# Kernel optimization log

Hardware: AMD Instinct MI355X
Metric: run time of the kernel (lower is better)

The kernel has to match this reference:

```python
import jax, jax.numpy as jnp
import numpy as np

B, T, DM, H, DK, N_STEPS = 4, 1024, 1024, 16, 64, 3


def setup_inputs() -> dict:
    key = jax.random.key(0)
    ks = jax.random.split(key, 8)
    s = 1.0 / np.sqrt(DM).astype(np.float32)
    x = jax.random.normal(ks[0], (B, T, DM), jnp.float32)
    W_Q = jax.random.normal(ks[1], (DM, DM), jnp.float32) * s
    W_K = jax.random.normal(ks[2], (DM, DM), jnp.float32) * s
    W_re = jax.random.normal(ks[3], (DM, DM), jnp.float32) * s
    W_im = jax.random.normal(ks[4], (DM, DM), jnp.float32) * s
    W_V = jax.random.normal(ks[5], (DM, DM), jnp.float32) * s
    W_O = jax.random.normal(ks[6], (DM, DM), jnp.float32) * s
    logit_lam = jnp.float32(0.0)  # sigmoid(0)=0.5 == cfg.lam
    return {"x": x, "W_Q": W_Q, "W_K": W_K, "W_re": W_re, "W_im": W_im,
            "W_V": W_V, "W_O": W_O, "logit_lam": logit_lam}


def _heads(y):
    # (B,T,DM) -> (B,H,T,DK)
    return y.reshape(B, T, H, DK).transpose(0, 2, 1, 3)


def reference(x, W_Q, W_K, W_re, W_im, W_V, W_O, logit_lam):
    # AdjacencyBuilder: soft row-normalized adjacency
    Q = _heads(x @ W_Q)
    K = _heads(x @ W_K)
    scores = jnp.einsum('bhtd,bhsd->bhts', Q, K) / jnp.float32(np.sqrt(DK))
    A = jax.nn.softmax(scores, axis=-1)                      # (B,H,T,T)
    # PhaseEncoding: complex oscillator versors
    D = jax.lax.complex(_heads(x @ W_re), _heads(x @ W_im))  # (B,H,T,DK) c64
    # TopologyPropagation: D <- (1-lam) D + lam A D, n_steps times
    lam = jax.nn.sigmoid(logit_lam)
    A_c = A.astype(jnp.complex64)
    for _ in range(N_STEPS):
        D = (1.0 - lam) * D + lam * jnp.einsum('bhts,bhsd->bhtd', A_c, D)
    # CollapseReadout (phase_align): softmax over T of cosine to mean field
    mean_D = jnp.mean(D, axis=-2, keepdims=True)             # (B,H,1,DK)
    dot = (D * jnp.conj(mean_D)).real
    norm = jnp.abs(D) * jnp.abs(mean_D) + 1e-8
    gate = jax.nn.softmax(dot / norm, axis=-2)               # (B,H,T,DK)
    # Value gating + output projection (dropout is identity in eval)
    V = _heads(x @ W_V)
    out = (gate * V).transpose(0, 2, 1, 3).reshape(B, T, DM) @ W_O
    return out, gate
```

## Files before the change

kernel.cpp:

```cpp
#include <hip/hip_runtime.h>
#include <math.h>

#define Bc 4
#define Tc 1024
#define DMc 1024
#define Hc 16
#define DKc 64
#define BHc 64
#define Mc 4096
#define TD (Tc*DKc)
#define TD2 (Tc*128)
#define TDS (128*2048)

typedef __bf16 bf16_t;
typedef bf16_t bf16x4 __attribute__((ext_vector_type(4)));
typedef bf16_t bf16x8 __attribute__((ext_vector_type(8)));
typedef float  f32x4  __attribute__((ext_vector_type(4)));

#define KLSTR 136
#define DLSTR 72

__device__ __forceinline__ bf16x8 ld8(const bf16_t* p) {
    return *(const bf16x8*)p;
}
__device__ __forceinline__ void packsplit4(bf16_t* dh, bf16_t* dl, float4 v) {
    bf16x4 h, l;
    h[0]=(bf16_t)v.x; l[0]=(bf16_t)(v.x-(float)h[0]);
    h[1]=(bf16_t)v.y; l[1]=(bf16_t)(v.y-(float)h[1]);
    h[2]=(bf16_t)v.z; l[2]=(bf16_t)(v.z-(float)h[2]);
    h[3]=(bf16_t)v.w; l[3]=(bf16_t)(v.w-(float)h[3]);
    *(bf16x4*)dh = h; *(bf16x4*)dl = l;
}
__device__ __forceinline__ unsigned pk2(bf16_t a, bf16_t b) {
    unsigned short ua = __builtin_bit_cast(unsigned short, a);
    unsigned short ub = __builtin_bit_cast(unsigned short, b);
    return (unsigned)ua | ((unsigned)ub << 16);
}
__device__ __forceinline__ void gload16(const bf16_t* g, bf16_t* l) {
    __builtin_amdgcn_global_load_lds(
        (__attribute__((address_space(1))) void*)(bf16_t*)g,
        (__attribute__((address_space(3))) void*)l, 16, 0, 0);
}

__global__ __launch_bounds__(256)
void convx_k(const float* __restrict__ x,
             bf16_t* __restrict__ xh, bf16_t* __restrict__ xl)
{
    size_t i = ((size_t)blockIdx.x * 256 + threadIdx.x) * 4;
    float4 v = *(const float4*)&x[i];
    packsplit4(&xh[i], &xl[i], v);
}

__global__ __launch_bounds__(256)
void convw_k(const float* __restrict__ W0, const float* __restrict__ W1,
             const float* __restrict__ W2, const float* __restrict__ W3,
             const float* __restrict__ W4, const float* __restrict__ W5,
             bf16_t* __restrict__ WT)
{
    __shared__ float tile[32][33];
    const float* Ws[6] = {W0, W1, W2, W3, W4, W5};
    const int wi = blockIdx.z;
    const float* W = Ws[wi];
    bf16_t* WTh = WT + (size_t)wi * 2097152;
    bf16_t* WTl = WTh + 1048576;

    const int tx = threadIdx.x & 31, ty = threadIdx.x >> 5;
    const int k0 = blockIdx.x * 32, n0 = blockIdx.y * 32;
#pragma unroll
    for (int i = 0; i < 4; i++)
        tile[ty + 8*i][tx] = W[(size_t)(k0 + ty + 8*i) * DMc + n0 + tx];
    __syncthreads();
    const int kg = threadIdx.x & 7, n = threadIdx.x >> 3;
    float4 v = make_float4(tile[kg*4+0][n], tile[kg*4+1][n],
                           tile[kg*4+2][n], tile[kg*4+3][n]);
    const size_t o = (size_t)(n0 + n) * DMc + k0 + kg*4;
    packsplit4(&WTh[o], &WTl[o], v);
}

template<int MODE>
__global__ __launch_bounds__(256)
void mgemm_k(const bf16_t* __restrict__ Ah, const bf16_t* __restrict__ Al,
             const bf16_t* __restrict__ WT,
             bf16_t* __restrict__ Oq, bf16_t* __restrict__ Ok,
             bf16_t* __restrict__ Od, float* __restrict__ Ov,
             float* __restrict__ Of)
{
    __shared__ bf16_t S[4][128*32];

    const int tid = threadIdx.x;
    const int wv  = tid >> 6;
    const int ln  = tid & 63;
    const int l15 = ln & 15;
    const int qd  = ln >> 4;
    const int m0  = blockIdx.x * 128;
    const int by  = blockIdx.y;

    const bf16_t *Bh, *Bl;
    int n0, sel, kt0, kt1;
    float* Opart;
    if (MODE == 0) {
        sel = by >> 3;
        n0 = (by & 7) * 128;
        Bh = WT + (size_t)sel * 2097152;
        Bl = Bh + 1048576;
        kt0 = 0; kt1 = DMc;
        Opart = nullptr;
    } else {
        sel = 5;
        Bh = WT + (size_t)5 * 2097152;
        Bl = Bh + 1048576;
        n0 = by * 128;
        kt0 = blockIdx.z * 256; kt1 = kt0 + 256;
        Opart = Of + (size_t)blockIdx.z * ((size_t)Mc * DMc);
    }

    const int srow = ln >> 2;
    const int scol = (ln & 3) * 8;
    const bf16_t* sbase;
    if (wv == 0)      sbase = Ah + (size_t)(m0 + srow) * DMc + scol;
    else if (wv == 1) sbase = Al + (size_t)(m0 + srow) * DMc + scol;
    else if (wv == 2) sbase = Bh + (size_t)(n0 + srow) * DMc + scol;
    else              sbase = Bl + (size_t)(n0 + srow) * DMc + scol;
    sbase += kt0;
    bf16_t* ldst = &S[wv][0];

    f32x4 acc[4][4];
#pragma unroll
    for (int i = 0; i < 4; i++)
#pragma unroll
        for (int j = 0; j < 4; j++) acc[i][j] = (f32x4)0.f;

#pragma unroll 1
    for (int kt = kt0; kt < kt1; kt += 32) {
        __syncthreads();
#pragma unroll
        for (int i = 0; i < 8; i++)
            gload16(sbase + (size_t)i * 16 * DMc, ldst + i * 512);
        sbase += 32;
        __syncthreads();

        bf16x8 fah[4], fal[4], fbh[4], fbl[4];
#pragma unroll
        for (int it = 0; it < 4; it++) {
            const int row = ((wv>>1)*64 + it*16 + l15) * 32 + qd*8;
            fah[it] = *(const bf16x8*)&S[0][row];
            fal[it] = *(const bf16x8*)&S[1][row];
        }
#pragma unroll
        for (int jt = 0; jt < 4; jt++) {
            const int row = ((wv&1)*64 + jt*16 + l15) * 32 + qd*8;
            fbh[jt] = *(const bf16x8*)&S[2][row];
            fbl[jt] = *(const bf16x8*)&S[3][row];
        }
#pragma unroll
        for (int it = 0; it < 4; it++)
#pragma unroll
            for (int jt = 0; jt < 4; jt++) {
                acc[it][jt] = __builtin_amdgcn_mfma_f32_16x16x32_bf16(
                    fah[it], fbh[jt], acc[it][jt], 0, 0, 0);
                acc[it][jt] = __builtin_amdgcn_mfma_f32_16x16x32_bf16(
                    fah[it], fbl[jt], acc[it][jt], 0, 0, 0);
                acc[it][jt] = __builtin_amdgcn_mfma_f32_16x16x32_bf16(
                    fal[it], fbh[jt], acc[it][jt], 0, 0, 0);
            }
    }

#pragma unroll
    for (int it = 0; it < 4; it++) {
        const int mb = m0 + (wv>>1)*64 + it*16 + qd*4;
#pragma unroll
        for (int jt = 0; jt < 4; jt++) {
            const int col = n0 + (wv&1)*64 + jt*16 + l15;
            if (MODE == 0) {
                const int hh = col >> 6;
                const int b  = mb >> 10, t0 = mb & 1023;
                if (sel <= 1) {
                    bf16_t* O = sel ? Ok : Oq;
                    const int d = col & 63;
#pragma unroll
                    for (int r = 0; r < 4; r++) {
                        const float val = acc[it][jt][r];
                        const size_t o = ((size_t)(b*Hc + hh)*Tc + t0 + r)*128 + d;
                        bf16_t vh = (bf16_t)val;
                        O[o]      = vh;
                        O[o + 64] = (bf16_t)(val - (float)vh);
                    }
                } else if (sel <= 3) {
                    const int d = (sel == 3 ? 64 : 0) + (col & 63);
                    bf16x4 h4, l4;
#pragma unroll
                    for (int r = 0; r < 4; r++) {
                        const float val = acc[it][jt][r];
                        h4[r] = (bf16_t)val;
                        l4[r] = (bf16_t)(val - (float)h4[r]);
                    }
                    const size_t o = (size_t)(b*Hc + hh)*TDS + (size_t)d*2048 + t0;
                    *(bf16x4*)&Od[o]        = h4;
                    *(bf16x4*)&Od[o + 1024] = l4;
                } else {
#pragma unroll
                    for (int r = 0; r < 4; r++)
                        Ov[((size_t)(b*Hc + hh)*Tc + t0 + r)*64 + (col & 63)]
                            = acc[it][jt][r];
                }
            } else {
#pragma unroll
                for (int r = 0; r < 4; r++)
                    Opart[(size_t)(mb + r) * DMc + col] = acc[it][jt][r];
            }
        }
    }
}

__global__ __launch_bounds__(256)
void reduce4_k(const float* __restrict__ p0, const float* __restrict__ p1,
               const float* __restrict__ p2, const float* __restrict__ p3,
               float* __restrict__ out)
{
    size_t i = ((size_t)blockIdx.x * 256 + threadIdx.x) * 4;
    float4 a = *(const float4*)&p0[i];
    float4 b = *(const float4*)&p1[i];
    float4 c = *(const float4*)&p2[i];
    float4 d = *(const float4*)&p3[i];
    *(float4*)&out[i] = make_float4(a.x+b.x+c.x+d.x, a.y+b.y+c.y+d.y,
                                    a.z+b.z+c.z+d.z, a.w+b.w+c.w+d.w);
}

template<int FINAL>
__global__ __launch_bounds__(256)
void prop_k(const bf16_t* __restrict__ Qg, const bf16_t* __restrict__ Kg,
            const bf16_t* __restrict__ DTin, bf16_t* __restrict__ DTout,
            float* __restrict__ Dc, const float* __restrict__ llam)
{
    __shared__ bf16_t Ks[32*KLSTR];
    __shared__ bf16_t Ds[128*DLSTR];

    const int tid = threadIdx.x;
    const int wv  = tid >> 6;
    const int ln  = tid & 63;
    const int l15 = ln & 15;
    const int qd  = ln >> 4;
    const int bh  = blockIdx.x;
    const int Tw  = blockIdx.y * 128 + wv * 32;

    const bf16_t* Qh  = Qg   + (size_t)bh * (Tc*128);
    const bf16_t* Kh  = Kg   + (size_t)bh * (Tc*128);
    const bf16_t* DTh = DTin + (size_t)bh * TDS;

    bf16x8 qfh[2][2], qfl[2][2];
#pragma unroll
    for (int tj = 0; tj < 2; tj++) {
        const bf16_t* qp = &Qh[(size_t)(Tw + tj*16 + l15) * 128];
#pragma unroll
        for (int ks = 0; ks < 2; ks++) {
            qfh[tj][ks] = *(const bf16x8*)&qp[ks*32 + qd*8];
            qfl[tj][ks] = *(const bf16x8*)&qp[64 + ks*32 + qd*8];
        }
    }

    const int idk0 = tid, idk1 = tid + 256;
    const bf16_t* srcK0 = Kh + (size_t)(idk0 >> 4) * 128 + (idk0 & 15) * 8;
    const bf16_t* srcK1 = Kh + (size_t)(idk1 >> 4) * 128 + (idk1 & 15) * 8;
    bf16_t* dstK0 = &Ks[(idk0 >> 4) * KLSTR + (idk0 & 15) * 8];
    bf16_t* dstK1 = &Ks[(idk1 >> 4) * KLSTR + (idk1 & 15) * 8];
    const bf16_t* srcD[4];
    bf16_t* dstD[4];
#pragma unroll
    for (int i = 0; i < 4; i++) {
        const int id = tid + i * 256;
        const int r = id >> 3, sg = id & 7;
        srcD[i] = DTh + (size_t)r * 2048
                      + (sg < 4 ? sg * 8 : 1024 + (sg - 4) * 8);
        dstD[i] = (sg < 4) ? &Ds[r * DLSTR + sg * 8]
                           : &Ds[r * DLSTR + 32 + (sg - 4) * 8];
    }
    bf16x8 kr0 = *(const bf16x8*)srcK0;
    bf16x8 kr1 = *(const bf16x8*)srcK1;
    bf16x8 dr[4];
#pragma unroll
    for (int i = 0; i < 4; i++) dr[i] = *(const bf16x8*)srcD[i];

    f32x4 acc[8][2];
#pragma unroll
    for (int i = 0; i < 8; i++)
#pragma unroll
        for (int j = 0; j < 2; j++) acc[i][j] = (f32x4)0.f;
    float rs[2] = {0.f, 0.f};

    const int srcA = (((qd & 1) * 2)     << 4) | l15;
    const int srcB = (((qd & 1) * 2 + 1) << 4) | l15;
    const bool loQuad = (qd < 2);

#pragma unroll 1
    for (int ch = 0; ch < 32; ch++) {
        __syncthreads();
        *(bf16x8*)dstK0 = kr0;
        *(bf16x8*)dstK1 = kr1;
#pragma unroll
        for (int i = 0; i < 4; i++) *(bf16x8*)dstD[i] = dr[i];
        __syncthreads();
        if (ch < 31) {
            kr0 = *(const bf16x8*)(srcK0 + (size_t)(ch + 1) * 4096);
            kr1 = *(const bf16x8*)(srcK1 + (size_t)(ch + 1) * 4096);
#pragma unroll
            for (int i = 0; i < 4; i++)
                dr[i] = *(const bf16x8*)(srcD[i] + (size_t)(ch + 1) * 32);
        }
        bf16x8 kfh[2][2], kfl[2][2];
#pragma unroll
        for (int si = 0; si < 2; si++) {
            const int row = (si*16 + l15) * KLSTR;
#pragma unroll
            for (int ks = 0; ks < 2; ks++) {
                kfh[si][ks] = ld8(&Ks[row + ks*32 + qd*8]);
                kfl[si][ks] = ld8(&Ks[row + 64 + ks*32 + qd*8]);
            }
        }
        f32x4 pacc[2][2];
#pragma unroll
        for (int si = 0; si < 2; si++)
#pragma unroll
            for (int tj = 0; tj < 2; tj++) pacc[si][tj] = (f32x4)0.f;
#pragma unroll
        for (int ks = 0; ks < 2; ks++)
#pragma unroll
            for (int si = 0; si < 2; si++)
#pragma unroll
                for (int tj = 0; tj < 2; tj++) {
                    pacc[si][tj] = __builtin_amdgcn_mfma_f32_16x16x32_bf16(
                        kfh[si][ks], qfh[tj][ks], pacc[si][tj], 0, 0, 0);
                    pacc[si][tj] = __builtin_amdgcn_mfma_f32_16x16x32_bf16(
                        kfl[si][ks], qfh[tj][ks], pacc[si][tj], 0, 0, 0);
                    pacc[si][tj] = __builtin_amdgcn_mfma_f32_16x16x32_bf16(
                        kfh[si][ks], qfl[tj][ks], pacc[si][tj], 0, 0, 0);
                }
        unsigned pk01h[2][2], pk23h[2][2], pk01l[2][2], pk23l[2][2];
#pragma unroll
        for (int si = 0; si < 2; si++)
#pragma unroll
            for (int tj = 0; tj < 2; tj++) {
                float e0 = __expf(pacc[si][tj][0] * 0.125f);
                float e1 = __expf(pacc[si][tj][1] * 0.125f);
                float e2 = __expf(pacc[si][tj][2] * 0.125f);
                float e3 = __expf(pacc[si][tj][3] * 0.125f);
                rs[tj] += (e0 + e1) + (e2 + e3);
                bf16_t h0=(bf16_t)e0, h1=(bf16_t)e1, h2=(bf16_t)e2, h3=(bf16_t)e3;
                pk01h[si][tj] = pk2(h0, h1);
                pk23h[si][tj] = pk2(h2, h3);
                pk01l[si][tj] = pk2((bf16_t)(e0-(float)h0), (bf16_t)(e1-(float)h1));
                pk23l[si][tj] = pk2((bf16_t)(e2-(float)h2), (bf16_t)(e3-(float)h3));
            }
        bf16x8 pfh[2], pfl[2];
#pragma unroll
        for (int tj = 0; tj < 2; tj++) {
            union { bf16x8 v; unsigned u[4]; } H, L;
            unsigned a0 = __shfl((int)pk01h[0][tj], srcA, 64);
            unsigned a1 = __shfl((int)pk23h[0][tj], srcA, 64);
            unsigned a2 = __shfl((int)pk01h[0][tj], srcB, 64);
            unsigned a3 = __shfl((int)pk23h[0][tj], srcB, 64);
            unsigned b0 = __shfl((int)pk01h[1][tj], srcA, 64);
            unsigned b1 = __shfl((int)pk23h[1][tj], srcA, 64);
            unsigned b2 = __shfl((int)pk01h[1][tj], srcB, 64);
            unsigned b3 = __shfl((int)pk23h[1][tj], srcB, 64);
            H.u[0] = loQuad ? a0 : b0;  H.u[1] = loQuad ? a1 : b1;
            H.u[2] = loQuad ? a2 : b2;  H.u[3] = loQuad ? a3 : b3;
            unsigned c0 = __shfl((int)pk01l[0][tj], srcA, 64);
            unsigned c1 = __shfl((int)pk23l[0][tj], srcA, 64);
            unsigned c2 = __shfl((int)pk01l[0][tj], srcB, 64);
            unsigned c3 = __shfl((int)pk23l[0][tj], srcB, 64);
            unsigned d0_ = __shfl((int)pk01l[1][tj], srcA, 64);
            unsigned d1 = __shfl((int)pk23l[1][tj], srcA, 64);
            unsigned d2 = __shfl((int)pk01l[1][tj], srcB, 64);
            unsigned d3 = __shfl((int)pk23l[1][tj], srcB, 64);
            L.u[0] = loQuad ? c0 : d0_; L.u[1] = loQuad ? c1 : d1;
            L.u[2] = loQuad ? c2 : d2;  L.u[3] = loQuad ? c3 : d3;
            pfh[tj] = H.v; pfl[tj] = L.v;
        }
#pragma unroll
        for (int half = 0; half < 2; half++) {
            bf16x8 dfh[4], dfl[4];
#pragma unroll
            for (int i = 0; i < 4; i++) {
                const int row = ((half*4 + i)*16 + l15) * DLSTR;
                dfh[i] = ld8(&Ds[row + qd*8]);
                dfl[i] = ld8(&Ds[row + 32 + qd*8]);
            }
#pragma unroll
            for (int i = 0; i < 4; i++)
#pragma unroll
                for (int tj = 0; tj < 2; tj++) {
                    acc[half*4+i][tj] = __builtin_amdgcn_mfma_f32_16x16x32_bf16(
                        dfh[i], pfh[tj], acc[half*4+i][tj], 0, 0, 0);
                    acc[half*4+i][tj] = __builtin_amdgcn_mfma_f32_16x16x32_bf16(
                        dfh[i], pfl[tj], acc[half*4+i][tj], 0, 0, 0);
                    acc[half*4+i][tj] = __builtin_amdgcn_mfma_f32_16x16x32_bf16(
                        dfl[i], pfh[tj], acc[half*4+i][tj], 0, 0, 0);
                }
        }
    }

#pragma unroll
    for (int tj = 0; tj < 2; tj++) {
        rs[tj] += __shfl_xor(rs[tj], 16);
        rs[tj] += __shfl_xor(rs[tj], 32);
    }

    const float lam = 1.f / (1.f + __expf(-llam[0]));
    const float oml = 1.f - lam;
    bf16_t* DToutg = (FINAL ? (bf16_t*)nullptr : DTout + (size_t)bh * TDS);

#pragma unroll
    for (int tj = 0; tj < 2; tj++) {
        const int t = Tw + tj*16 + l15;
        const float s = lam / rs[tj];
#pragma unroll
        for (int it = 0; it < 8; it++) {
            const int d0 = it*16 + qd*4;
            float v[4];
#pragma unroll
            for (int r = 0; r < 4; r++) {
                const size_t ro = (size_t)(d0 + r)*2048 + t;
                float res = (float)DTh[ro] + (float)DTh[ro + 1024];
                v[r] = oml*res + s*acc[it][tj][r];
            }
            if (FINAL) {
                *(float4*)&Dc[((size_t)bh*Tc + t)*128 + d0] =
                    make_float4(v[0], v[1], v[2], v[3]);
            } else {
#pragma unroll
                for (int r = 0; r < 4; r++) {
                    const size_t ro = (size_t)(d0 + r)*2048 + t;
                    bf16_t h = (bf16_t)v[r];
                    DToutg[ro]        = h;
                    DToutg[ro + 1024] = (bf16_t)(v[r] - (float)h);
                }
            }
        }
    }
}

__global__ __launch_bounds__(256)
void mean1_k(const float* __restrict__ D,
             float* __restrict__ M1re, float* __restrict__ M1im)
{
    __shared__ float sre[4][64], sim[4][64];
    const int bh = blockIdx.x, y = blockIdx.y;
    const int d = threadIdx.x & 63, q = threadIdx.x >> 6;
    const float* p = D + (size_t)bh * TD2;
    float ar = 0.f, ai = 0.f;
    const int t0 = y*128 + q*32;
    for (int t = t0; t < t0 + 32; t++) {
        ar += p[t*128 + d]; ai += p[t*128 + 64 + d];
    }
    sre[q][d] = ar; sim[q][d] = ai;
    __syncthreads();
    if (threadIdx.x < 64) {
        M1re[(bh*8 + y)*64 + d] = sre[0][d]+sre[1][d]+sre[2][d]+sre[3][d];
        M1im[(bh*8 + y)*64 + d] = sim[0][d]+sim[1][d]+sim[2][d]+sim[3][d];
    }
}

__global__ __launch_bounds__(64)
void mean2_k(const float* __restrict__ M1re, const float* __restrict__ M1im,
             float* __restrict__ Mre, float* __restrict__ Mim)
{
    const int bh = blockIdx.x, d = threadIdx.x;
    float r = 0.f, im = 0.f;
    for (int y = 0; y < 8; y++) {
        r  += M1re[(bh*8 + y)*64 + d];
        im += M1im[(bh*8 + y)*64 + d];
    }
    Mre[bh*64 + d] = r  * (1.f/1024.f);
    Mim[bh*64 + d] = im * (1.f/1024.f);
}

__global__ __launch_bounds__(256)
void gate1_k(const float* __restrict__ D,
             const float* __restrict__ Mre, const float* __restrict__ Mim,
             float* __restrict__ Gp)
{
    __shared__ float part[4][64];
    const int bh = blockIdx.x, y = blockIdx.y;
    const int d = threadIdx.x & 63, q = threadIdx.x >> 6;
    const float* p = D + (size_t)bh * TD2;
    const float mre = Mre[bh*64 + d], mim = Mim[bh*64 + d];
    const float mabs = sqrtf(mre*mre + mim*mim);

    float ps = 0.f;
    const int t0 = y*128 + q*32;
    for (int t = t0; t < t0 + 32; t++) {
        float dr = p[t*128 + d], dv = p[t*128 + 64 + d];
        float c = (dr*mre + dv*mim) / (sqrtf(dr*dr + dv*dv)*mabs + 1e-8f);
        ps += __expf(c);
    }
    part[q][d] = ps;
    __syncthreads();
    if (threadIdx.x < 64)
        Gp[(bh*8 + y)*64 + d] = part[0][d]+part[1][d]+part[2][d]+part[3][d];
}

__global__ __launch_bounds__(256)
void gate2_k(const float* __restrict__ D,
             const float* __restrict__ Mre, const float* __restrict__ Mim,
             const float* __restrict__ V, const float* __restrict__ Gp,
             float* __restrict__ gate_out,
             bf16_t* __restrict__ gVh, bf16_t* __restrict__ gVl)
{
    __shared__ float dinv[64];
    const int bh = blockIdx.x, y = blockIdx.y;
    const int d = threadIdx.x & 63, q = threadIdx.x >> 6;
    if (threadIdx.x < 64) {
        float s = 0.f;
        for (int yy = 0; yy < 8; yy++) s += Gp[(bh*8 + yy)*64 + d];
        dinv[d] = 1.f / s;
    }
    __syncthreads();

    const float* p = D + (size_t)bh * TD2;
    const float mre = Mre[bh*64 + d], mim = Mim[bh*64 + d];
    const float mabs = sqrtf(mre*mre + mim*mim);
    const float di_ = dinv[d];
    const int b = bh >> 4, hh = bh & 15;
    const float* pv = V + (size_t)bh * TD;
    const int t0 = y*128 + q*32;
    for (int t = t0; t < t0 + 32; t++) {
        float dr = p[t*128 + d], dv = p[t*128 + 64 + d];
        float c = (dr*mre + dv*mim) / (sqrtf(dr*dr + dv*dv)*mabs + 1e-8f);
        float g = __expf(c) * di_;
        gate_out[(size_t)bh*TD + t*64 + d] = g;
        float gv = g * pv[t*64 + d];
        size_t o = ((size_t)b*Tc + t)*DMc + hh*64 + d;
        bf16_t gh = (bf16_t)gv;
        gVh[o] = gh;
        gVl[o] = (bf16_t)(gv - (float)gh);
    }
}

extern "C" void kernel_launch(void* const* d_in, const int* in_sizes, int n_in,
                              void* d_out, int out_size, void* d_ws, size_t ws_size,
                              hipStream_t stream)
{
    const float* x    = (const float*)d_in[0];
    const float* W_Q  = (const float*)d_in[1];
    const float* W_K  = (const float*)d_in[2];
    const float* W_re = (const float*)d_in[3];
    const float* W_im = (const float*)d_in[4];
    const float* W_V  = (const float*)d_in[5];
    const float* W_O  = (const float*)d_in[6];
    const float* llam = (const float*)d_in[7];

    float* out      = (float*)d_out;
    float* gate_out = out + (size_t)Mc * DMc;

    float* ws = (float*)d_ws;
    const size_t M1 = 1024*1024;
    float*  Dc  = ws;
    bf16_t* DT1 = (bf16_t*)ws;
    bf16_t* DT0 = (bf16_t*)(ws + 8*M1);
    float*  V   = ws + 16*M1;
    bf16_t* Qs  = (bf16_t*)(ws + 20*M1);
    bf16_t* Ksb = (bf16_t*)(ws + 24*M1);
    float*  Mre = ws + 28*M1;
    float*  Mim = Mre + 4096;
    bf16_t* xh  = (bf16_t*)(ws + 28*M1 + 8192);
    bf16_t* xl  = xh + 4*M1;
    bf16_t* WT  = xl + 4*M1;
    bf16_t* gVh = xh;
    bf16_t* gVl = xl;
    float* Gp   = ws + 24*M1;
    float* M1re = Gp + 32768;
    float* M1im = M1re + 32768;
    float* P0 = ws + 8*M1;
    float* P1 = ws + 12*M1;
    float* P2 = ws + 16*M1;
    float* P3 = ws + 20*M1;

    convx_k<<<4096, 256, 0, stream>>>(x, xh, xl);
    convw_k<<<dim3(32, 32, 6), 256, 0, stream>>>(
        W_Q, W_K, W_re, W_im, W_V, W_O, WT);

    mgemm_k<0><<<dim3(32, 40), 256, 0, stream>>>(
        xh, xl, WT, Qs, Ksb, DT0, V, nullptr);

    prop_k<0><<<dim3(64, 8), 256, 0, stream>>>(Qs, Ksb, DT0, DT1, nullptr, llam);
    prop_k<0><<<dim3(64, 8), 256, 0, stream>>>(Qs, Ksb, DT1, DT0, nullptr, llam);
    prop_k<1><<<dim3(64, 8), 256, 0, stream>>>(Qs, Ksb, DT0, nullptr, Dc, llam);

    mean1_k<<<dim3(64, 8), 256, 0, stream>>>(Dc, M1re, M1im);
    mean2_k<<<64, 64, 0, stream>>>(M1re, M1im, Mre, Mim);
    gate1_k<<<dim3(64, 8), 256, 0, stream>>>(Dc, Mre, Mim, Gp);
    gate2_k<<<dim3(64, 8), 256, 0, stream>>>(Dc, Mre, Mim, V, Gp,
                                             gate_out, gVh, gVl);

    mgemm_k<1><<<dim3(32, 8, 4), 256, 0, stream>>>(
        gVh, gVl, WT, nullptr, nullptr, nullptr, nullptr, P0);
    reduce4_k<<<4096, 256, 0, stream>>>(P0, P1, P2, P3, out);
}
```

Baseline: 608.3 us.

## Load K and D fragments directly from global memory, dropping LDS staging

The propagation kernel no longer stages K and D tiles through shared memory with register prefetch and two barriers per chunk. Each wave now loads its MFMA operand fragments straight from global memory, relying on L1/L2 caching for the reuse across the four waves of a block. This removes barrier and LDS traffic, but it adds redundant global loads per wave and drops the software prefetch, which exposes load latency.

```diff
diff --git a/kernel.cpp b/kernel.cpp
--- a/kernel.cpp
+++ b/kernel.cpp
@@ -17,12 +17,6 @@
 typedef bf16_t bf16x8 __attribute__((ext_vector_type(8)));
 typedef float  f32x4  __attribute__((ext_vector_type(4)));
 
-#define KLSTR 136
-#define DLSTR 72
-
-__device__ __forceinline__ bf16x8 ld8(const bf16_t* p) {
-    return *(const bf16x8*)p;
-}
 __device__ __forceinline__ void packsplit4(bf16_t* dh, bf16_t* dl, float4 v) {
     bf16x4 h, l;
     h[0]=(bf16_t)v.x; l[0]=(bf16_t)(v.x-(float)h[0]);
@@ -232,9 +226,6 @@
             const bf16_t* __restrict__ DTin, bf16_t* __restrict__ DTout,
             float* __restrict__ Dc, const float* __restrict__ llam)
 {
-    __shared__ bf16_t Ks[32*KLSTR];
-    __shared__ bf16_t Ds[128*DLSTR];
-
     const int tid = threadIdx.x;
     const int wv  = tid >> 6;
     const int ln  = tid & 63;
@@ -258,27 +249,8 @@
         }
     }
 
-    const int idk0 = tid, idk1 = tid + 256;
-    const bf16_t* srcK0 = Kh + (size_t)(idk0 >> 4) * 128 + (idk0 & 15) * 8;
-    const bf16_t* srcK1 = Kh + (size_t)(idk1 >> 4) * 128 + (idk1 & 15) * 8;
-    bf16_t* dstK0 = &Ks[(idk0 >> 4) * KLSTR + (idk0 & 15) * 8];
-    bf16_t* dstK1 = &Ks[(idk1 >> 4) * KLSTR + (idk1 & 15) * 8];
-    const bf16_t* srcD[4];
-    bf16_t* dstD[4];
-#pragma unroll
-    for (int i = 0; i < 4; i++) {
-        const int id = tid + i * 256;
-        const int r = id >> 3, sg = id & 7;
-        srcD[i] = DTh + (size_t)r * 2048
-                      + (sg < 4 ? sg * 8 : 1024 + (sg - 4) * 8);
-        dstD[i] = (sg < 4) ? &Ds[r * DLSTR + sg * 8]
-                           : &Ds[r * DLSTR + 32 + (sg - 4) * 8];
-    }
-    bf16x8 kr0 = *(const bf16x8*)srcK0;
-    bf16x8 kr1 = *(const bf16x8*)srcK1;
-    bf16x8 dr[4];
-#pragma unroll
-    for (int i = 0; i < 4; i++) dr[i] = *(const bf16x8*)srcD[i];
+    const bf16_t* kbase = Kh + (size_t)l15 * 128 + qd * 8;
+    const bf16_t* dbase = DTh + (size_t)l15 * 2048 + qd * 8;
 
     f32x4 acc[8][2];
 #pragma unroll
@@ -293,27 +265,15 @@
 
 #pragma unroll 1
     for (int ch = 0; ch < 32; ch++) {
-        __syncthreads();
-        *(bf16x8*)dstK0 = kr0;
-        *(bf16x8*)dstK1 = kr1;
-#pragma unroll
-        for (int i = 0; i < 4; i++) *(bf16x8*)dstD[i] = dr[i];
-        __syncthreads();
-        if (ch < 31) {
-            kr0 = *(const bf16x8*)(srcK0 + (size_t)(ch + 1) * 4096);
-            kr1 = *(const bf16x8*)(srcK1 + (size_t)(ch + 1) * 4096);
-#pragma unroll
-            for (int i = 0; i < 4; i++)
-                dr[i] = *(const bf16x8*)(srcD[i] + (size_t)(ch + 1) * 32);
-        }
+        const int s0 = ch * 32;
         bf16x8 kfh[2][2], kfl[2][2];
 #pragma unroll
         for (int si = 0; si < 2; si++) {
-            const int row = (si*16 + l15) * KLSTR;
+            const bf16_t* kp = kbase + (size_t)(s0 + si*16) * 128;
 #pragma unroll
             for (int ks = 0; ks < 2; ks++) {
-                kfh[si][ks] = ld8(&Ks[row + ks*32 + qd*8]);
-                kfl[si][ks] = ld8(&Ks[row + 64 + ks*32 + qd*8]);
+                kfh[si][ks] = *(const bf16x8*)(kp + ks*32);
+                kfl[si][ks] = *(const bf16x8*)(kp + 64 + ks*32);
             }
         }
         f32x4 pacc[2][2];
@@ -381,9 +341,9 @@
             bf16x8 dfh[4], dfl[4];
 #pragma unroll
             for (int i = 0; i < 4; i++) {
-                const int row = ((half*4 + i)*16 + l15) * DLSTR;
-                dfh[i] = ld8(&Ds[row + qd*8]);
-                dfl[i] = ld8(&Ds[row + 32 + qd*8]);
+                const bf16_t* dp = dbase + (size_t)(half*4 + i) * (16*2048) + s0;
+                dfh[i] = *(const bf16x8*)dp;
+                dfl[i] = *(const bf16x8*)(dp + 1024);
             }
 #pragma unroll
             for (int i = 0; i < 4; i++)
```

Result: slower. 933.2 us (+53.4%).
